# Kernel tuning notes

Measured on AMD Instinct MI355X. Metric: run time of the kernel, lower is better.

The kernel has to match this reference:

```python
import jax, jax.numpy as jnp
import numpy as np

C_IN, C_OUT, KH, KW = 64, 128, 3, 3
STRIDE, PAD, DIL = 1, 1, 1
EPS = 1e-5


def setup_inputs() -> dict:
    key = jax.random.key(0)
    ks = jax.random.split(key, 7)
    B, H, W = 8, 112, 112
    x = jax.random.normal(ks[0], (B, C_IN, H, W), dtype=jnp.float32)
    # offset conv: produces 2*KH*KW offset channels; small init keeps offsets sane
    w_off = jax.random.normal(ks[1], (2 * KH * KW, C_IN, KH, KW), dtype=jnp.float32) * 0.01
    b_off = jax.random.normal(ks[2], (2 * KH * KW,), dtype=jnp.float32) * 0.01
    # deformable conv weight/bias
    fan_in = C_IN * KH * KW
    w_dcn = jax.random.normal(ks[3], (C_OUT, C_IN, KH, KW), dtype=jnp.float32) / np.sqrt(fan_in)
    b_dcn = jax.random.normal(ks[4], (C_OUT,), dtype=jnp.float32) * 0.01
    gamma = jnp.ones((C_OUT,), dtype=jnp.float32)
    beta = jnp.zeros((C_OUT,), dtype=jnp.float32)
    return {"x": x, "w_off": w_off, "b_off": b_off, "w_dcn": w_dcn,
            "b_dcn": b_dcn, "gamma": gamma, "beta": beta}


def _conv2d(x, w, b):
    y = jax.lax.conv_general_dilated(
        x, w, window_strides=(STRIDE, STRIDE),
        padding=((PAD, PAD), (PAD, PAD)),
        rhs_dilation=(DIL, DIL),
        dimension_numbers=("NCHW", "OIHW", "NCHW"))
    return y + b[None, :, None, None]


def _deform_conv(x, offset, w, b):
    # x: [B,C,H,W]; offset: [B, 2*KH*KW, Ho, Wo] with (dy, dx) pairs per tap
    B, C, H, W = x.shape
    KK = KH * KW
    Ho, Wo = offset.shape[2], offset.shape[3]
    off = offset.reshape(B, KK, 2, Ho, Wo)
    ky = (jnp.arange(KK) // KW).astype(jnp.float32)  # kernel row per tap
    kx = (jnp.arange(KK) % KW).astype(jnp.float32)
    base_y = (jnp.arange(Ho) * STRIDE - PAD).astype(jnp.float32)
    base_x = (jnp.arange(Wo) * STRIDE - PAD).astype(jnp.float32)
    # sampling positions [B, KK, Ho, Wo]
    py = off[:, :, 0] + base_y[None, None, :, None] + (ky * DIL)[None, :, None, None]
    px = off[:, :, 1] + base_x[None, None, None, :] + (kx * DIL)[None, :, None, None]

    y0 = jnp.floor(py)
    x0 = jnp.floor(px)
    wy1 = py - y0  # weight for y0+1
    wx1 = px - x0
    y0i = y0.astype(jnp.int32)
    x0i = x0.astype(jnp.int32)

    x_flat = x.reshape(B, C, H * W)

    def gather_corner(yi, xi, wgt):
        # yi, xi, wgt: [B, KK, Ho, Wo]
        valid = (yi >= 0) & (yi < H) & (xi >= 0) & (xi < W)
        idx = jnp.clip(yi, 0, H - 1) * W + jnp.clip(xi, 0, W - 1)
        idx = idx.reshape(B, -1)  # [B, KK*Ho*Wo]
        vals = jnp.take_along_axis(x_flat, idx[:, None, :], axis=2)  # [B, C, N]
        coef = (wgt * valid.astype(wgt.dtype)).reshape(B, 1, -1)
        return vals * coef

    samp = (gather_corner(y0i,     x0i,     (1 - wy1) * (1 - wx1))
            + gather_corner(y0i,     x0i + 1, (1 - wy1) * wx1)
            + gather_corner(y0i + 1, x0i,     wy1 * (1 - wx1))
            + gather_corner(y0i + 1, x0i + 1, wy1 * wx1))
    samp = samp.reshape(B, C, KK, Ho, Wo)
    out = jnp.einsum("bckhw,ock->bohw", samp, w.reshape(w.shape[0], C, KK))
    return out + b[None, :, None, None]


def reference(x, w_off, b_off, w_dcn, b_dcn, gamma, beta):
    offset = _conv2d(x, w_off, b_off)
    y = _deform_conv(x, offset, w_dcn, b_dcn)
    # BatchNorm2d (training mode: biased batch stats) + ReLU
    mean = jnp.mean(y, axis=(0, 2, 3))
    var = jnp.var(y, axis=(0, 2, 3))
    yhat = (y - mean[None, :, None, None]) * jax.lax.rsqrt(var + EPS)[None, :, None, None]
    y = gamma[None, :, None, None] * yhat + beta[None, :, None, None]
    return jax.nn.relu(y)
```

## Files before the change

kernel.cpp:

```cpp
#include <hip/hip_runtime.h>

#define H    112
#define W    112
#define HW   12544
#define CIN  64
#define COUT 128
#define BATCH 8
#define KK   9
#define OFFC 18
#define EPS  1e-5f
#define TP   32
#define KDIM 576
#define KPAD 584

typedef unsigned short ushort;
typedef unsigned int uint;
typedef __attribute__((ext_vector_type(8))) short short8;
typedef __attribute__((ext_vector_type(8))) ushort ushort8;
typedef __attribute__((ext_vector_type(4))) float floatx4;

__device__ __forceinline__ ushort f2bf(float f) {
  uint u = __float_as_uint(f);
  u = (u + 0x7FFFu + ((u >> 16) & 1u)) >> 16;
  return (ushort)u;
}

__device__ __forceinline__ uint pack_bf2(float f0, float f1) {
  uint u0 = __float_as_uint(f0) + 0x8000u;
  uint u1 = __float_as_uint(f1) + 0x8000u;
  return __builtin_amdgcn_perm(u1, u0, 0x07060302u);
}

__device__ __forceinline__ float bf2f(ushort u) {
  return __uint_as_float(((uint)u) << 16);
}

__global__ __launch_bounds__(256) void k_transpose_x(
    const float* __restrict__ x, ushort* __restrict__ xTb) {
  __shared__ float tile[64][65];
  int b = blockIdx.y;
  int p0 = blockIdx.x * 64;
  int tid = threadIdx.x;
  int j = tid & 63, cb = tid >> 6;
#pragma unroll
  for (int i = 0; i < 16; ++i) {
    int ci = cb * 16 + i;
    tile[ci][j] = x[((size_t)(b * CIN + ci)) * HW + p0 + j];
  }
  __syncthreads();
  int px = tid >> 2, ciq = tid & 3;
  uint pk[4];
#pragma unroll
  for (int g = 0; g < 4; ++g) {
    int ci = ciq * 16 + g * 4;
    pk[g] = 0;
    uint lo = pack_bf2(tile[ci + 0][px], tile[ci + 1][px]);
    uint hi = pack_bf2(tile[ci + 2][px], tile[ci + 3][px]);
    ((uint2*)pk)[g >> 1] = make_uint2(0, 0);
    pk[g] = lo;
    *(uint2*)&xTb[((size_t)b * HW + p0 + px) * 64 + ci] = make_uint2(lo, hi);
  }
}

__global__ __launch_bounds__(256) void k_prep_w(
    const float* __restrict__ w_off, const float* __restrict__ w_dcn,
    float* __restrict__ w_r, ushort* __restrict__ w_mf) {
  int i = blockIdx.x * 256 + threadIdx.x;
  if (i < OFFC * KDIM) {
    int oc = i / KDIM, rem = i - oc * KDIM;
    int ci = rem / KK, kk = rem - ci * KK;
    w_r[(kk * 64 + ci) * OFFC + oc] = w_off[i];
  } else if (i < OFFC * KDIM + COUT * KDIM) {
    int jj = i - OFFC * KDIM;
    int co = jj / KDIM, rem = jj - co * KDIM;
    int ci = rem / KK, kk = rem - ci * KK;
    w_mf[co * KDIM + kk * 64 + ci] = f2bf(w_dcn[jj]);
  }
}

__global__ __launch_bounds__(256) void k_offset_conv(
    const ushort* __restrict__ xTb, const float* __restrict__ w_r,
    const float* __restrict__ bias, float* __restrict__ out) {
  int b = blockIdx.y;
  int p = blockIdx.x * 256 + threadIdx.x;
  int ho = p / W, wo = p - ho * W;
  float acc[OFFC];
#pragma unroll
  for (int oc = 0; oc < OFFC; ++oc) acc[oc] = bias[oc];
  const ushort* xb = xTb + (size_t)b * HW * 64;
  for (int t = 0; t < 9; ++t) {
    int yy = ho + t / 3 - 1;
    int xx = wo + t % 3 - 1;
    bool valid = (yy >= 0) & (yy < H) & (xx >= 0) & (xx < W);
    const ushort8* src = (const ushort8*)(xb + ((size_t)(yy * W + xx) << 6));
    const float* wbase = w_r + t * 64 * OFFC;
    if (valid) {
#pragma unroll 2
      for (int cg = 0; cg < 8; ++cg) {
        ushort8 v = src[cg];
#pragma unroll
        for (int jj = 0; jj < 8; ++jj) {
          float xv = bf2f(v[jj]);
          const float* wp = wbase + (cg * 8 + jj) * OFFC;
#pragma unroll
          for (int oc = 0; oc < OFFC; ++oc)
            acc[oc] = fmaf(xv, wp[oc], acc[oc]);
        }
      }
    }
  }
#pragma unroll
  for (int oc = 0; oc < OFFC; ++oc)
    out[((size_t)b * OFFC + oc) * HW + p] = acc[oc];
}

__global__ __launch_bounds__(256) void k_deform(
    const ushort* __restrict__ xTb, const float* __restrict__ off,
    const ushort* __restrict__ w_mf, float* __restrict__ y) {
  __shared__ float4 s_w[KK][TP];
  __shared__ int4   s_i[KK][TP];
  __shared__ ushort samp[TP][KPAD];

  int b = blockIdx.y;
  int p0 = blockIdx.x * TP;
  int tid = threadIdx.x;
  const ushort* xb = xTb + (size_t)b * HW * 64;

  for (int it = tid; it < KK * TP; it += 256) {
    int kk = it >> 5;
    int px = it & 31;
    int p = p0 + px;
    int ho = p / W, wo = p - ho * W;
    float dy = off[((size_t)b * OFFC + 2 * kk) * HW + p];
    float dx = off[((size_t)b * OFFC + 2 * kk + 1) * HW + p];
    float py = dy + (float)(ho - 1 + kk / 3);
    float pxx = dx + (float)(wo - 1 + kk % 3);
    float y0f = floorf(py), x0f = floorf(pxx);
    float wy1 = py - y0f, wx1 = pxx - x0f;
    int y0 = (int)y0f, x0 = (int)x0f;
    int y1 = y0 + 1, x1 = x0 + 1;
    float vy0 = (y0 >= 0 && y0 < H) ? 1.f : 0.f;
    float vy1 = (y1 >= 0 && y1 < H) ? 1.f : 0.f;
    float vx0 = (x0 >= 0 && x0 < W) ? 1.f : 0.f;
    float vx1 = (x1 >= 0 && x1 < W) ? 1.f : 0.f;
    int cy0 = min(max(y0, 0), H - 1), cy1 = min(max(y1, 0), H - 1);
    int cx0 = min(max(x0, 0), W - 1), cx1 = min(max(x1, 0), W - 1);
    s_w[kk][px] = make_float4((1.f - wy1) * (1.f - wx1) * vy0 * vx0,
                              (1.f - wy1) * wx1 * vy0 * vx1,
                              wy1 * (1.f - wx1) * vy1 * vx0,
                              wy1 * wx1 * vy1 * vx1);
    s_i[kk][px] = make_int4((cy0 * W + cx0) << 6, (cy0 * W + cx1) << 6,
                            (cy1 * W + cx0) << 6, (cy1 * W + cx1) << 6);
  }
  __syncthreads();

#pragma unroll
  for (int r = 0; r < 9; ++r) {
    int it = tid + r * 256;
    int px = it / 72;
    int rem = it - px * 72;
    int kk = rem >> 3;
    int cig = rem & 7;
    int ci0 = cig * 8;
    float4 wv = s_w[kk][px];
    int4 iv = s_i[kk][px];
    ushort8 c0 = *(const ushort8*)(xb + iv.x + ci0);
    ushort8 c1 = *(const ushort8*)(xb + iv.y + ci0);
    ushort8 c2 = *(const ushort8*)(xb + iv.z + ci0);
    ushort8 c3 = *(const ushort8*)(xb + iv.w + ci0);
    uint pk[4];
#pragma unroll
    for (int g = 0; g < 4; ++g) {
      float r0 = wv.x * bf2f(c0[2 * g])     + wv.y * bf2f(c1[2 * g]) +
                 wv.z * bf2f(c2[2 * g])     + wv.w * bf2f(c3[2 * g]);
      float r1 = wv.x * bf2f(c0[2 * g + 1]) + wv.y * bf2f(c1[2 * g + 1]) +
                 wv.z * bf2f(c2[2 * g + 1]) + wv.w * bf2f(c3[2 * g + 1]);
      pk[g] = pack_bf2(r0, r1);
    }
    *(uint4*)&samp[px][kk * 64 + ci0] = make_uint4(pk[0], pk[1], pk[2], pk[3]);
  }
  __syncthreads();

  int wave = tid >> 6, lane = tid & 63;
  int row16 = lane & 15, quad = lane >> 4;
  int koff = quad * 8;
  int co_base = wave * 32;
  const ushort* wa0 = w_mf + (size_t)(co_base + row16) * KDIM + koff;
  const ushort* wa1 = w_mf + (size_t)(co_base + 16 + row16) * KDIM + koff;
  const ushort* sb0 = &samp[row16][koff];
  const ushort* sb1 = &samp[16 + row16][koff];

  floatx4 acc00 = {0.f, 0.f, 0.f, 0.f}, acc01 = acc00, acc10 = acc00, acc11 = acc00;
#pragma unroll
  for (int ks = 0; ks < KDIM / 32; ++ks) {
    short8 A0 = *(const short8*)(wa0 + ks * 32);
    short8 A1 = *(const short8*)(wa1 + ks * 32);
    short8 B0 = *(const short8*)(sb0 + ks * 32);
    short8 B1 = *(const short8*)(sb1 + ks * 32);
    acc00 = __builtin_amdgcn_mfma_f32_16x16x32_bf16(A0, B0, acc00, 0, 0, 0);
    acc01 = __builtin_amdgcn_mfma_f32_16x16x32_bf16(A0, B1, acc01, 0, 0, 0);
    acc10 = __builtin_amdgcn_mfma_f32_16x16x32_bf16(A1, B0, acc10, 0, 0, 0);
    acc11 = __builtin_amdgcn_mfma_f32_16x16x32_bf16(A1, B1, acc11, 0, 0, 0);
  }

  float* yb = y + (size_t)b * COUT * HW + p0;
#pragma unroll
  for (int reg = 0; reg < 4; ++reg) {
    int r0 = quad * 4 + reg;
    yb[(size_t)(co_base + r0) * HW + row16]      = acc00[reg];
    yb[(size_t)(co_base + r0) * HW + 16 + row16] = acc01[reg];
    yb[(size_t)(co_base + 16 + r0) * HW + row16]      = acc10[reg];
    yb[(size_t)(co_base + 16 + r0) * HW + 16 + row16] = acc11[reg];
  }
}

__global__ __launch_bounds__(256) void k_stats(const float* __restrict__ y,
                                               float* __restrict__ stats) {
  int c = blockIdx.x & 127;
  int half = blockIdx.x >> 7;
  int tid = threadIdx.x;
  float s = 0.f, s2 = 0.f;
#pragma unroll
  for (int bb = 0; bb < 2; ++bb) {
    int b = half * 2 + bb;
    const float4* yp = (const float4*)(y + ((size_t)b * COUT + c) * HW);
    for (int p = tid; p < HW / 4; p += 256) {
      float4 v = yp[p];
      s += v.x + v.y + v.z + v.w;
      s2 += v.x * v.x + v.y * v.y + v.z * v.z + v.w * v.w;
    }
  }
#pragma unroll
  for (int o = 32; o > 0; o >>= 1) {
    s += __shfl_down(s, o, 64);
    s2 += __shfl_down(s2, o, 64);
  }
  __shared__ float ls[4], ls2[4];
  int lane = tid & 63, wid = tid >> 6;
  if (lane == 0) { ls[wid] = s; ls2[wid] = s2; }
  __syncthreads();
  if (tid == 0) {
    atomicAdd(&stats[c], ls[0] + ls[1] + ls[2] + ls[3]);
    atomicAdd(&stats[COUT + c], ls2[0] + ls2[1] + ls2[2] + ls2[3]);
  }
}

__global__ __launch_bounds__(256) void k_norm(const float* __restrict__ y,
                                              const float* __restrict__ stats,
                                              const float* __restrict__ gamma,
                                              const float* __restrict__ beta,
                                              float* __restrict__ out) {
  int i4 = blockIdx.x * 256 + threadIdx.x;
  const int total4 = BATCH * COUT * HW / 4;
  if (i4 >= total4) return;
  size_t i = (size_t)i4 * 4;
  int c = (int)((i / HW) & (COUT - 1));
  const float N = (float)(BATCH * HW);
  float m = stats[c] / N;
  float var = stats[COUT + c] / N - m * m;
  float r = rsqrtf(var + EPS);
  float g = gamma[c], bt = beta[c];
  float4 v = *(const float4*)&y[i];
  v.x = fmaxf(0.f, (v.x - m) * r * g + bt);
  v.y = fmaxf(0.f, (v.y - m) * r * g + bt);
  v.z = fmaxf(0.f, (v.z - m) * r * g + bt);
  v.w = fmaxf(0.f, (v.w - m) * r * g + bt);
  *(float4*)&out[i] = v;
}

extern "C" void kernel_launch(void* const* d_in, const int* in_sizes, int n_in,
                              void* d_out, int out_size, void* d_ws, size_t ws_size,
                              hipStream_t stream) {
  const float* x     = (const float*)d_in[0];
  const float* w_off = (const float*)d_in[1];
  const float* b_off = (const float*)d_in[2];
  const float* w_dcn = (const float*)d_in[3];
  const float* gamma = (const float*)d_in[5];
  const float* beta  = (const float*)d_in[6];
  float* out = (float*)d_out;

  float* ws = (float*)d_ws;
  float*  off_buf = ws;
  float*  w_r     = off_buf + 1806336;
  float*  y       = w_r + 10368;
  float*  stats   = y + 12845056;
  ushort* xTb     = (ushort*)(stats + 256);
  ushort* w_mf    = xTb + 6422528;

  hipMemsetAsync(stats, 0, 256 * sizeof(float), stream);
  k_transpose_x<<<dim3(HW / 64, BATCH), 256, 0, stream>>>(x, xTb);
  k_prep_w<<<(OFFC * KDIM + COUT * KDIM + 255) / 256, 256, 0, stream>>>(w_off, w_dcn, w_r, w_mf);
  k_offset_conv<<<dim3(HW / 256, BATCH), 256, 0, stream>>>(xTb, w_r, b_off, off_buf);
  k_deform<<<dim3(HW / TP, BATCH), 256, 0, stream>>>(xTb, off_buf, w_mf, y);
  k_stats<<<512, 256, 0, stream>>>(y, stats);
  k_norm<<<(BATCH * COUT * HW / 4 + 255) / 256, 256, 0, stream>>>(y, stats, gamma, beta, out);
}
```

Measured before the change: 243.3 us.

## Move offset conv to bf16 MFMA and split deform sampling into K halves

Rewrites the offset convolution from a scalar fp32 FMA loop to bf16 MFMA tiles, with the 18 output channels padded to 32 and the weights pre-packed in bf16. This lowers the precision of the offset computation. The deform kernel now builds the sampled tile in two channel halves, each followed by half of the MFMA K loop, which halves shared memory per block and could raise occupancy. The price is an extra barrier and reordered weight packing.

```diff
diff --git a/kernel.cpp b/kernel.cpp
--- a/kernel.cpp
+++ b/kernel.cpp
@@ -11,7 +11,8 @@
 #define EPS  1e-5f
 #define TP   32
 #define KDIM 576
-#define KPAD 584
+#define KHALF 288
+#define KPAD2 296
 
 typedef unsigned short ushort;
 typedef unsigned int uint;
@@ -49,69 +50,74 @@
   }
   __syncthreads();
   int px = tid >> 2, ciq = tid & 3;
-  uint pk[4];
 #pragma unroll
   for (int g = 0; g < 4; ++g) {
     int ci = ciq * 16 + g * 4;
-    pk[g] = 0;
     uint lo = pack_bf2(tile[ci + 0][px], tile[ci + 1][px]);
     uint hi = pack_bf2(tile[ci + 2][px], tile[ci + 3][px]);
-    ((uint2*)pk)[g >> 1] = make_uint2(0, 0);
-    pk[g] = lo;
     *(uint2*)&xTb[((size_t)b * HW + p0 + px) * 64 + ci] = make_uint2(lo, hi);
   }
 }
 
 __global__ __launch_bounds__(256) void k_prep_w(
     const float* __restrict__ w_off, const float* __restrict__ w_dcn,
-    float* __restrict__ w_r, ushort* __restrict__ w_mf) {
+    ushort* __restrict__ w_offT, ushort* __restrict__ w_mf) {
   int i = blockIdx.x * 256 + threadIdx.x;
-  if (i < OFFC * KDIM) {
-    int oc = i / KDIM, rem = i - oc * KDIM;
-    int ci = rem / KK, kk = rem - ci * KK;
-    w_r[(kk * 64 + ci) * OFFC + oc] = w_off[i];
-  } else if (i < OFFC * KDIM + COUT * KDIM) {
-    int jj = i - OFFC * KDIM;
-    int co = jj / KDIM, rem = jj - co * KDIM;
-    int ci = rem / KK, kk = rem - ci * KK;
-    w_mf[co * KDIM + kk * 64 + ci] = f2bf(w_dcn[jj]);
+  if (i < 32 * KDIM) {
+    int oc = i / KDIM, k = i - oc * KDIM;
+    int kk = k >> 6, ci = k & 63;
+    float v = (oc < OFFC) ? w_off[(oc * CIN + ci) * KK + kk] : 0.f;
+    w_offT[i] = f2bf(v);
+  } else if (i < 32 * KDIM + COUT * KDIM) {
+    int jj = i - 32 * KDIM;
+    int co = jj / KDIM, k = jj - co * KDIM;
+    int h = k / KHALF, r = k - h * KHALF;
+    int kk = r >> 5, cil = r & 31;
+    int ci = h * 32 + cil;
+    w_mf[jj] = f2bf(w_dcn[(co * CIN + ci) * KK + kk]);
   }
 }
 
 __global__ __launch_bounds__(256) void k_offset_conv(
-    const ushort* __restrict__ xTb, const float* __restrict__ w_r,
+    const ushort* __restrict__ xTb, const ushort* __restrict__ w_offT,
     const float* __restrict__ bias, float* __restrict__ out) {
   int b = blockIdx.y;
-  int p = blockIdx.x * 256 + threadIdx.x;
+  int wave = threadIdx.x >> 6, lane = threadIdx.x & 63;
+  int row16 = lane & 15, quad = lane >> 4;
+  int p = blockIdx.x * 64 + wave * 16 + row16;
   int ho = p / W, wo = p - ho * W;
-  float acc[OFFC];
-#pragma unroll
-  for (int oc = 0; oc < OFFC; ++oc) acc[oc] = bias[oc];
   const ushort* xb = xTb + (size_t)b * HW * 64;
-  for (int t = 0; t < 9; ++t) {
-    int yy = ho + t / 3 - 1;
-    int xx = wo + t % 3 - 1;
+
+  short8 Bf[18];
+#pragma unroll
+  for (int ks = 0; ks < 18; ++ks) {
+    int kk = ks >> 1;
+    int ci0 = (ks & 1) * 32 + quad * 8;
+    int kh = kk / 3, kw = kk - kh * 3;
+    int yy = ho + kh - 1, xx = wo + kw - 1;
     bool valid = (yy >= 0) & (yy < H) & (xx >= 0) & (xx < W);
-    const ushort8* src = (const ushort8*)(xb + ((size_t)(yy * W + xx) << 6));
-    const float* wbase = w_r + t * 64 * OFFC;
-    if (valid) {
-#pragma unroll 2
-      for (int cg = 0; cg < 8; ++cg) {
-        ushort8 v = src[cg];
-#pragma unroll
-        for (int jj = 0; jj < 8; ++jj) {
-          float xv = bf2f(v[jj]);
-          const float* wp = wbase + (cg * 8 + jj) * OFFC;
-#pragma unroll
-          for (int oc = 0; oc < OFFC; ++oc)
-            acc[oc] = fmaf(xv, wp[oc], acc[oc]);
-        }
-      }
-    }
-  }
-#pragma unroll
-  for (int oc = 0; oc < OFFC; ++oc)
-    out[((size_t)b * OFFC + oc) * HW + p] = acc[oc];
+    short8 v = {0, 0, 0, 0, 0, 0, 0, 0};
+    if (valid) v = *(const short8*)(xb + ((size_t)(yy * W + xx) << 6) + ci0);
+    Bf[ks] = v;
+  }
+  floatx4 acc0 = {0.f, 0.f, 0.f, 0.f}, acc1 = acc0;
+  const ushort* wa0 = w_offT + row16 * KDIM + quad * 8;
+  const ushort* wa1 = w_offT + (16 + row16) * KDIM + quad * 8;
+#pragma unroll
+  for (int ks = 0; ks < 18; ++ks) {
+    short8 A0 = *(const short8*)(wa0 + ks * 32);
+    short8 A1 = *(const short8*)(wa1 + ks * 32);
+    acc0 = __builtin_amdgcn_mfma_f32_16x16x32_bf16(A0, Bf[ks], acc0, 0, 0, 0);
+    acc1 = __builtin_amdgcn_mfma_f32_16x16x32_bf16(A1, Bf[ks], acc1, 0, 0, 0);
+  }
+  float* ob = out + (size_t)b * OFFC * HW;
+#pragma unroll
+  for (int reg = 0; reg < 4; ++reg) {
+    int oc = quad * 4 + reg;
+    ob[(size_t)oc * HW + p] = acc0[reg] + bias[oc];
+    int oc1 = 16 + oc;
+    if (oc1 < OFFC) ob[(size_t)oc1 * HW + p] = acc1[reg] + bias[oc1];
+  }
 }
 
 __global__ __launch_bounds__(256) void k_deform(
@@ -119,7 +125,7 @@
     const ushort* __restrict__ w_mf, float* __restrict__ y) {
   __shared__ float4 s_w[KK][TP];
   __shared__ int4   s_i[KK][TP];
-  __shared__ ushort samp[TP][KPAD];
+  __shared__ ushort samp[TP][KPAD2];
 
   int b = blockIdx.y;
   int p0 = blockIdx.x * TP;
@@ -154,53 +160,62 @@
   }
   __syncthreads();
 
-#pragma unroll
-  for (int r = 0; r < 9; ++r) {
-    int it = tid + r * 256;
-    int px = it / 72;
-    int rem = it - px * 72;
-    int kk = rem >> 3;
-    int cig = rem & 7;
-    int ci0 = cig * 8;
-    float4 wv = s_w[kk][px];
-    int4 iv = s_i[kk][px];
-    ushort8 c0 = *(const ushort8*)(xb + iv.x + ci0);
-    ushort8 c1 = *(const ushort8*)(xb + iv.y + ci0);
-    ushort8 c2 = *(const ushort8*)(xb + iv.z + ci0);
-    ushort8 c3 = *(const ushort8*)(xb + iv.w + ci0);
-    uint pk[4];
-#pragma unroll
-    for (int g = 0; g < 4; ++g) {
-      float r0 = wv.x * bf2f(c0[2 * g])     + wv.y * bf2f(c1[2 * g]) +
-                 wv.z * bf2f(c2[2 * g])     + wv.w * bf2f(c3[2 * g]);
-      float r1 = wv.x * bf2f(c0[2 * g + 1]) + wv.y * bf2f(c1[2 * g + 1]) +
-                 wv.z * bf2f(c2[2 * g + 1]) + wv.w * bf2f(c3[2 * g + 1]);
-      pk[g] = pack_bf2(r0, r1);
-    }
-    *(uint4*)&samp[px][kk * 64 + ci0] = make_uint4(pk[0], pk[1], pk[2], pk[3]);
-  }
-  __syncthreads();
-
   int wave = tid >> 6, lane = tid & 63;
   int row16 = lane & 15, quad = lane >> 4;
   int koff = quad * 8;
   int co_base = wave * 32;
   const ushort* wa0 = w_mf + (size_t)(co_base + row16) * KDIM + koff;
   const ushort* wa1 = w_mf + (size_t)(co_base + 16 + row16) * KDIM + koff;
-  const ushort* sb0 = &samp[row16][koff];
-  const ushort* sb1 = &samp[16 + row16][koff];
 
   floatx4 acc00 = {0.f, 0.f, 0.f, 0.f}, acc01 = acc00, acc10 = acc00, acc11 = acc00;
-#pragma unroll
-  for (int ks = 0; ks < KDIM / 32; ++ks) {
-    short8 A0 = *(const short8*)(wa0 + ks * 32);
-    short8 A1 = *(const short8*)(wa1 + ks * 32);
-    short8 B0 = *(const short8*)(sb0 + ks * 32);
-    short8 B1 = *(const short8*)(sb1 + ks * 32);
-    acc00 = __builtin_amdgcn_mfma_f32_16x16x32_bf16(A0, B0, acc00, 0, 0, 0);
-    acc01 = __builtin_amdgcn_mfma_f32_16x16x32_bf16(A0, B1, acc01, 0, 0, 0);
-    acc10 = __builtin_amdgcn_mfma_f32_16x16x32_bf16(A1, B0, acc10, 0, 0, 0);
-    acc11 = __builtin_amdgcn_mfma_f32_16x16x32_bf16(A1, B1, acc11, 0, 0, 0);
+
+  for (int h = 0; h < 2; ++h) {
+#pragma unroll
+    for (int r = 0; r < 5; ++r) {
+      int it = tid + r * 256;
+      if (it < 1152) {
+        int px = it / 36;
+        int rem = it - px * 36;
+        int kk = rem >> 2;
+        int cig = rem & 3;
+        int cil0 = cig * 8;
+        int cio = h * 32 + cil0;
+        float4 wv = s_w[kk][px];
+        int4 iv = s_i[kk][px];
+        ushort8 c0 = *(const ushort8*)(xb + iv.x + cio);
+        ushort8 c1 = *(const ushort8*)(xb + iv.y + cio);
+        ushort8 c2 = *(const ushort8*)(xb + iv.z + cio);
+        ushort8 c3 = *(const ushort8*)(xb + iv.w + cio);
+        uint pk[4];
+#pragma unroll
+        for (int g = 0; g < 4; ++g) {
+          float r0 = wv.x * bf2f(c0[2 * g])     + wv.y * bf2f(c1[2 * g]) +
+                     wv.z * bf2f(c2[2 * g])     + wv.w * bf2f(c3[2 * g]);
+          float r1 = wv.x * bf2f(c0[2 * g + 1]) + wv.y * bf2f(c1[2 * g + 1]) +
+                     wv.z * bf2f(c2[2 * g + 1]) + wv.w * bf2f(c3[2 * g + 1]);
+          pk[g] = pack_bf2(r0, r1);
+        }
+        *(uint4*)&samp[px][kk * 32 + cil0] = make_uint4(pk[0], pk[1], pk[2], pk[3]);
+      }
+    }
+    __syncthreads();
+
+    const ushort* sb0 = &samp[row16][koff];
+    const ushort* sb1 = &samp[16 + row16][koff];
+    const ushort* a0 = wa0 + h * KHALF;
+    const ushort* a1 = wa1 + h * KHALF;
+#pragma unroll
+    for (int ks = 0; ks < 9; ++ks) {
+      short8 A0 = *(const short8*)(a0 + ks * 32);
+      short8 A1 = *(const short8*)(a1 + ks * 32);
+      short8 B0 = *(const short8*)(sb0 + ks * 32);
+      short8 B1 = *(const short8*)(sb1 + ks * 32);
+      acc00 = __builtin_amdgcn_mfma_f32_16x16x32_bf16(A0, B0, acc00, 0, 0, 0);
+      acc01 = __builtin_amdgcn_mfma_f32_16x16x32_bf16(A0, B1, acc01, 0, 0, 0);
+      acc10 = __builtin_amdgcn_mfma_f32_16x16x32_bf16(A1, B0, acc10, 0, 0, 0);
+      acc11 = __builtin_amdgcn_mfma_f32_16x16x32_bf16(A1, B1, acc11, 0, 0, 0);
+    }
+    if (h == 0) __syncthreads();
   }
 
   float* yb = y + (size_t)b * COUT * HW + p0;
@@ -281,16 +296,16 @@
 
   float* ws = (float*)d_ws;
   float*  off_buf = ws;
-  float*  w_r     = off_buf + 1806336;
-  float*  y       = w_r + 10368;
+  float*  y       = off_buf + 1806336;
   float*  stats   = y + 12845056;
   ushort* xTb     = (ushort*)(stats + 256);
   ushort* w_mf    = xTb + 6422528;
+  ushort* w_offT  = w_mf + 73728;
 
   hipMemsetAsync(stats, 0, 256 * sizeof(float), stream);
   k_transpose_x<<<dim3(HW / 64, BATCH), 256, 0, stream>>>(x, xTb);
-  k_prep_w<<<(OFFC * KDIM + COUT * KDIM + 255) / 256, 256, 0, stream>>>(w_off, w_dcn, w_r, w_mf);
-  k_offset_conv<<<dim3(HW / 256, BATCH), 256, 0, stream>>>(xTb, w_r, b_off, off_buf);
+  k_prep_w<<<(32 * KDIM + COUT * KDIM + 255) / 256, 256, 0, stream>>>(w_off, w_dcn, w_offT, w_mf);
+  k_offset_conv<<<dim3(HW / 64, BATCH), 256, 0, stream>>>(xTb, w_offT, b_off, off_buf);
   k_deform<<<dim3(HW / TP, BATCH), 256, 0, stream>>>(xTb, off_buf, w_mf, y);
   k_stats<<<512, 256, 0, stream>>>(y, stats);
   k_norm<<<(BATCH * COUT * HW / 4 + 255) / 256, 256, 0, stream>>>(y, stats, gamma, beta, out);
```

Result: faster. 236.5 us (-2.8%).
